# Kernel tuning notes

Hardware: AMD Instinct MI355X
Metric: run time of the kernel (lower is better)

Reference implementation:

```python
import jax, jax.numpy as jnp
import numpy as np

NUM_HEADS = 12
EPS = 1e-6


def setup_inputs() -> dict:
    key = jax.random.key(0)
    k1, k2, k3, k4 = jax.random.split(key, 4)
    N, B, D = 1025, 8, 768
    x = jax.random.normal(k1, (N, B, D), dtype=jnp.float32)
    # torch nn.Linear weights: [out_features, in_features]
    w_qkv = jax.random.normal(k2, (3 * D, D), dtype=jnp.float32) * (D ** -0.5)
    w_proj = jax.random.normal(k3, (D, D), dtype=jnp.float32) * (D ** -0.5)
    b_proj = jax.random.normal(k4, (D,), dtype=jnp.float32) * 0.01
    return {"x": x, "w_qkv": w_qkv, "w_proj": w_proj, "b_proj": b_proj}


def reference(x, w_qkv, w_proj, b_proj):
    N, B, D = x.shape
    H = NUM_HEADS
    hd = D // H
    scale = hd ** -0.5
    scale_vv = scale * 1.0  # scale_multiplier = 1.0

    xb = jnp.transpose(x, (1, 0, 2))  # [B, N, D]
    qkv = xb @ w_qkv.T  # [B, N, 3D]
    qkv = qkv.reshape(B, N, 3, H, hd).transpose(2, 0, 3, 1, 4)  # [3, B, H, N, hd]
    q, k, v = qkv[0], qkv[1], qkv[2]

    # QK path: only row 0 of out_ori survives the masking, compute just that row
    scores0 = jnp.einsum('bhqd,bhkd->bhqk', q[:, :, :1], k) * scale  # [B,H,1,N]
    attn0 = jax.nn.softmax(scores0, axis=-1)
    out0 = jnp.einsum('bhqk,bhkd->bhqd', attn0, v)  # [B,H,1,hd]

    # VV cosine path: only rows 1: survive
    vn = v / jnp.maximum(jnp.linalg.norm(v, axis=-1, keepdims=True), EPS)
    scores_vv = jnp.einsum('bhqd,bhkd->bhqk', vn[:, :, 1:], vn) * scale_vv  # [B,H,N-1,N]
    attn_vv = jax.nn.softmax(scores_vv, axis=-1)
    out_vv = jnp.einsum('bhqk,bhkd->bhqd', attn_vv, v)  # [B,H,N-1,hd]

    out = jnp.concatenate([out0, out_vv], axis=2)  # [B,H,N,hd]
    out = out.transpose(0, 2, 1, 3).reshape(B, N, D)
    out = out @ w_proj.T + b_proj
    return jnp.transpose(out, (1, 0, 2))  # [N, B, D]
```

## Files before the change

kernel.cpp:

```cpp
#include <hip/hip_runtime.h>

typedef unsigned short u16;
typedef unsigned int   u32;
typedef __attribute__((ext_vector_type(8))) short short8;
typedef __attribute__((ext_vector_type(4))) float f32x4;

#define AS1 __attribute__((address_space(1)))
#define AS3 __attribute__((address_space(3)))

#define NSEQ  1025
#define BB    8
#define DD    768
#define HH    12
#define MROWS 8200
#define MPAD  8320
#define KPAD  1088

__device__ __forceinline__ void gl2lds16(const void* g, void* l) {
  __builtin_amdgcn_global_load_lds((const AS1 u32*)g, (AS3 u32*)l, 16, 0, 0);
}
__device__ __forceinline__ u16 f2bf(float f) {
  u32 u = __float_as_uint(f);
  return (u16)((u + 0x7FFFu + ((u >> 16) & 1u)) >> 16);
}
__device__ __forceinline__ float bf2f(u16 u) { return __uint_as_float(((u32)u) << 16); }

__global__ __launch_bounds__(256) void prep(const float* __restrict__ x,
                                            const float* __restrict__ wqkv,
                                            const float* __restrict__ wproj,
                                            u16* __restrict__ xb,
                                            u16* __restrict__ wkv,
                                            u16* __restrict__ wpj) {
  const int XB_G  = MPAD * 192;
  const int WKV_G = 1536 * 192;
  const int WPJ_G = 768 * 192;
  int g = blockIdx.x * 256 + threadIdx.x;
  float4 v;
  u16* dst;
  size_t di;
  if (g < XB_G) {
    int m = g / 192, e4 = g - m * 192;
    if (m < MROWS) {
      int bb = m / NSEQ, ns = m - bb * NSEQ;
      v = ((const float4*)x)[(size_t)(ns * BB + bb) * 192 + e4];
    } else {
      v.x = v.y = v.z = v.w = 0.f;
    }
    dst = xb; di = (size_t)g;
  } else if (g < XB_G + WKV_G) {
    int r = g - XB_G;
    v = ((const float4*)wqkv)[(size_t)147456 + r];
    dst = wkv; di = (size_t)r;
  } else if (g < XB_G + WKV_G + WPJ_G) {
    int r = g - XB_G - WKV_G;
    v = ((const float4*)wproj)[r];
    dst = wpj; di = (size_t)r;
  } else {
    return;
  }
  uint2 o;
  o.x = (u32)f2bf(v.x) | ((u32)f2bf(v.y) << 16);
  o.y = (u32)f2bf(v.z) | ((u32)f2bf(v.w) << 16);
  ((uint2*)dst)[di] = o;
}

template <int MODE, int NT>
__global__ __launch_bounds__(256) void gemm_bt(const u16* __restrict__ A,
                                               const u16* __restrict__ W,
                                               u16* __restrict__ Cbf,
                                               float* __restrict__ Cf,
                                               const float* __restrict__ bias,
                                               int ldc) {
  __shared__ u16 sA[128 * 64];
  __shared__ u16 sW[128 * 64];
  const int id = blockIdx.x;
  const int rx = id & 7, qx = id >> 3;
  const int kq = qx / NT;
  const int m_t = rx + (kq << 3);
  if (m_t > 64) return;
  const int n_t = qx - kq * NT;
  const int m0 = m_t << 7, n0 = n_t << 7;

  const int tid = threadIdx.x;
  const int w = tid >> 6, lane = tid & 63;
  const int wm = w & 1, wn = w >> 1;
  const int lc = lane & 15, lr = lane >> 4;

  f32x4 zero4 = {0.f, 0.f, 0.f, 0.f};
  f32x4 acc[4][4];
#pragma unroll
  for (int i = 0; i < 4; ++i)
#pragma unroll
    for (int j = 0; j < 4; ++j) acc[i][j] = zero4;

  const int r0 = tid >> 3;
  const int ko = (tid & 7) << 3;
  const u16* gA = A + (size_t)(m0 + r0) * DD + ko;
  const u16* gW = W + (size_t)(n0 + r0) * DD + ko;
  char* lA = (char*)sA + tid * 16;
  char* lW = (char*)sW + tid * 16;

#pragma unroll 1
  for (int kt = 0; kt < 12; ++kt) {
    __syncthreads();
#pragma unroll
    for (int j = 0; j < 4; ++j) {
      gl2lds16(gA + (size_t)j * 32 * DD + kt * 64, lA + j * 4096);
      gl2lds16(gW + (size_t)j * 32 * DD + kt * 64, lW + j * 4096);
    }
    __syncthreads();
#pragma unroll
    for (int kk = 0; kk < 2; ++kk) {
      short8 af[4], wf[4];
#pragma unroll
      for (int mt = 0; mt < 4; ++mt)
        af[mt] = *(const short8*)((char*)sA + ((wm << 6) + (mt << 4) + lc) * 128 + (kk << 6) + (lr << 4));
#pragma unroll
      for (int nt = 0; nt < 4; ++nt)
        wf[nt] = *(const short8*)((char*)sW + ((wn << 6) + (nt << 4) + lc) * 128 + (kk << 6) + (lr << 4));
#pragma unroll
      for (int mt = 0; mt < 4; ++mt)
#pragma unroll
        for (int nt = 0; nt < 4; ++nt)
          acc[mt][nt] = __builtin_amdgcn_mfma_f32_16x16x32_bf16(af[mt], wf[nt], acc[mt][nt], 0, 0, 0);
    }
  }

  if (MODE == 0) {
#pragma unroll
    for (int mt = 0; mt < 4; ++mt)
#pragma unroll
      for (int r = 0; r < 4; ++r) {
        int m = m0 + (wm << 6) + (mt << 4) + (lr << 2) + r;
        if (m < MROWS) {
          size_t base = (size_t)m * ldc + n0 + (wn << 6) + lc;
#pragma unroll
          for (int nt = 0; nt < 4; ++nt) Cbf[base + (nt << 4)] = f2bf(acc[mt][nt][r]);
        }
      }
  } else {
    float b4[4];
#pragma unroll
    for (int nt = 0; nt < 4; ++nt) b4[nt] = bias[n0 + (wn << 6) + (nt << 4) + lc];
#pragma unroll
    for (int mt = 0; mt < 4; ++mt)
#pragma unroll
      for (int r = 0; r < 4; ++r) {
        int m = m0 + (wm << 6) + (mt << 4) + (lr << 2) + r;
        if (m < MROWS) {
          int bb = m / NSEQ;
          int ns = m - bb * NSEQ;
          float* o = Cf + (size_t)ns * (BB * DD) + bb * DD + n0 + (wn << 6) + lc;
#pragma unroll
          for (int nt = 0; nt < 4; ++nt) o[nt << 4] = acc[mt][nt][r] + b4[nt];
        }
      }
  }
}

__global__ __launch_bounds__(256) void q0_kernel(const float* __restrict__ x,
                                                 const float* __restrict__ wq,
                                                 float* __restrict__ q0) {
  __shared__ float red[256];
  int bid = blockIdx.x;
  int b = bid / HH, c = bid - b * HH;
  int tid = threadIdx.x;
  int dp = (c << 6) + (tid >> 2), part = tid & 3;
  const float4* x4 = (const float4*)(x + (size_t)b * DD + part * 192);
  const float4* w4 = (const float4*)(wq + (size_t)dp * DD + part * 192);
  float acc = 0.f;
#pragma unroll 4
  for (int e = 0; e < 48; ++e) {
    float4 a = x4[e], w = w4[e];
    acc += a.x * w.x + a.y * w.y + a.z * w.z + a.w * w.w;
  }
  red[tid] = acc;
  __syncthreads();
  if (part == 0) q0[b * DD + dp] = red[tid] + red[tid + 1] + red[tid + 2] + red[tid + 3];
}

__global__ __launch_bounds__(256) void transpose_v(const u16* __restrict__ kv,
                                                   u16* __restrict__ vT,
                                                   u16* __restrict__ vn) {
  __shared__ u16 tile[64][72];
  __shared__ float red[256];
  __shared__ float sInv[64];
  int bid = blockIdx.x;
  int kc = bid % 17;
  int t2 = bid / 17;
  int h = t2 % HH, b = t2 / HH;
  int tid = threadIdx.x;
  int kl = tid >> 2, dc = (tid & 3) << 4;
  int key = kc * 64 + kl;
  u32 vals[8];
  if (key < NSEQ) {
    const u32* g = (const u32*)(kv + ((size_t)b * NSEQ + key) * 1536 + DD + h * 64 + dc);
#pragma unroll
    for (int i = 0; i < 8; ++i) vals[i] = g[i];
  } else {
#pragma unroll
    for (int i = 0; i < 8; ++i) vals[i] = 0;
  }
  float part = 0.f;
#pragma unroll
  for (int i = 0; i < 8; ++i) {
    float a = bf2f((u16)(vals[i] & 0xFFFF));
    float c = bf2f((u16)(vals[i] >> 16));
    part += a * a + c * c;
    ((u32*)&tile[kl][dc])[i] = vals[i];
  }
  red[tid] = part;
  __syncthreads();
  if ((tid & 3) == 0) {
    float s = red[tid] + red[tid + 1] + red[tid + 2] + red[tid + 3];
    sInv[kl] = (key < NSEQ) ? 1.0f / fmaxf(sqrtf(s), 1e-6f) : 0.0f;
  }
  __syncthreads();
  float iv = sInv[kl];
  u32 ovn[8];
#pragma unroll
  for (int i = 0; i < 8; ++i) {
    float a = bf2f((u16)(vals[i] & 0xFFFF)) * iv;
    float c = bf2f((u16)(vals[i] >> 16)) * iv;
    ovn[i] = (u32)f2bf(a) | ((u32)f2bf(c) << 16);
  }
  u32* on = (u32*)(vn + ((size_t)(b * HH + h) * KPAD + key) * 64 + dc);
#pragma unroll
  for (int i = 0; i < 8; ++i) on[i] = ovn[i];
  int dl = tid >> 2, ks = (tid & 3) << 4;
  u32 ov[8];
#pragma unroll
  for (int i = 0; i < 8; ++i)
    ov[i] = (u32)tile[ks + 2 * i][dl] | ((u32)tile[ks + 2 * i + 1][dl] << 16);
  u16* o = vT + (size_t)(b * HH + h) * 64 * KPAD + (size_t)dl * KPAD + kc * 64 + ks;
#pragma unroll
  for (int i = 0; i < 8; ++i) ((u32*)o)[i] = ov[i];
}

__global__ __launch_bounds__(256) void row0_attn(const float* __restrict__ q0,
                                                 const u16* __restrict__ kv,
                                                 u16* __restrict__ attn) {
  __shared__ float sq[64];
  __shared__ float sc[NSEQ];
  __shared__ float red[256];
  __shared__ float rpv[32][68];
  int bid = blockIdx.x;
  int b = bid / HH, h = bid - b * HH;
  int tid = threadIdx.x;
  if (tid < 64) sq[tid] = q0[b * DD + h * 64 + tid];
  __syncthreads();
  float mx = -1e30f;
  for (int n = tid; n < NSEQ; n += 256) {
    const u32* kr = (const u32*)(kv + ((size_t)b * NSEQ + n) * 1536 + h * 64);
    float s = 0.f;
#pragma unroll
    for (int i = 0; i < 32; ++i) {
      u32 u = kr[i];
      s += bf2f((u16)(u & 0xFFFF)) * sq[2 * i] + bf2f((u16)(u >> 16)) * sq[2 * i + 1];
    }
    s *= 0.125f;
    sc[n] = s;
    mx = fmaxf(mx, s);
  }
  red[tid] = mx;
  __syncthreads();
  for (int st = 128; st > 0; st >>= 1) {
    if (tid < st) red[tid] = fmaxf(red[tid], red[tid + st]);
    __syncthreads();
  }
  mx = red[0];
  __syncthreads();
  float ds = 0.f;
  for (int n = tid; n < NSEQ; n += 256) {
    float p = __expf(sc[n] - mx);
    sc[n] = p;
    ds += p;
  }
  red[tid] = ds;
  __syncthreads();
  for (int st = 128; st > 0; st >>= 1) {
    if (tid < st) red[tid] += red[tid + st];
    __syncthreads();
  }
  float den = red[0];
  __syncthreads();

  int kp = tid >> 3, dc = (tid & 7) << 3;
  const u16* vb = kv + (size_t)b * NSEQ * 1536 + DD + h * 64 + dc;
  float acc[8];
#pragma unroll
  for (int i = 0; i < 8; ++i) acc[i] = 0.f;
#pragma unroll 4
  for (int j = 0; j < 32; ++j) {
    int n = kp + (j << 5);
    uint4 v = *(const uint4*)(vb + (size_t)n * 1536);
    float p = sc[n];
    acc[0] += p * bf2f((u16)(v.x & 0xFFFF));
    acc[1] += p * bf2f((u16)(v.x >> 16));
    acc[2] += p * bf2f((u16)(v.y & 0xFFFF));
    acc[3] += p * bf2f((u16)(v.y >> 16));
    acc[4] += p * bf2f((u16)(v.z & 0xFFFF));
    acc[5] += p * bf2f((u16)(v.z >> 16));
    acc[6] += p * bf2f((u16)(v.w & 0xFFFF));
    acc[7] += p * bf2f((u16)(v.w >> 16));
  }
  if (kp == 0) {
    uint4 v = *(const uint4*)(vb + (size_t)1024 * 1536);
    float p = sc[1024];
    acc[0] += p * bf2f((u16)(v.x & 0xFFFF));
    acc[1] += p * bf2f((u16)(v.x >> 16));
    acc[2] += p * bf2f((u16)(v.y & 0xFFFF));
    acc[3] += p * bf2f((u16)(v.y >> 16));
    acc[4] += p * bf2f((u16)(v.z & 0xFFFF));
    acc[5] += p * bf2f((u16)(v.z >> 16));
    acc[6] += p * bf2f((u16)(v.w & 0xFFFF));
    acc[7] += p * bf2f((u16)(v.w >> 16));
  }
#pragma unroll
  for (int i = 0; i < 8; ++i) rpv[kp][dc + i] = acc[i];
  __syncthreads();
  if (tid < 64) {
    float s = 0.f;
#pragma unroll
    for (int p = 0; p < 32; ++p) s += rpv[p][tid];
    attn[(size_t)b * NSEQ * DD + h * 64 + tid] = f2bf(s / den);
  }
}

__global__ __launch_bounds__(256) void vv_attn(const u16* __restrict__ vn,
                                               const u16* __restrict__ vT,
                                               u16* __restrict__ attn) {
  __shared__ u16 sQ[2 * 128 * 32];
  __shared__ u16 sK[2 * 64 * 32];
  __shared__ u16 sV[2 * 64 * 32];
  __shared__ u16 sP[128 * 72];

  const int tid = threadIdx.x, w = tid >> 6, lane = tid & 63;
  const int lc = lane & 15, lr = lane >> 4;
  const int bh = blockIdx.x;
  const int m0 = blockIdx.y << 7;
  const int b = bh / HH, h = bh - b * HH;
  const char* nb = (const char*)(vn + (size_t)bh * KPAD * 64);
  const char* tb = (const char*)(vT + (size_t)bh * 64 * KPAD);

#pragma unroll
  for (int j = 0; j < 4; ++j) {
    int lin = (w << 12) + (j << 10) + (lane << 4);
    int hf = lin >> 13, r = (lin >> 6) & 127, off = lin & 63;
    gl2lds16(nb + (size_t)(1 + m0 + r) * 128 + hf * 64 + off, (char*)sQ + lin);
  }

  f32x4 zero4 = {0.f, 0.f, 0.f, 0.f};
  f32x4 oacc[2][4];
  f32x4 dacc[2];
#pragma unroll
  for (int i = 0; i < 2; ++i) {
    dacc[i] = zero4;
#pragma unroll
    for (int j = 0; j < 4; ++j) oacc[i][j] = zero4;
  }
  short8 ones;
#pragma unroll
  for (int i = 0; i < 8; ++i) ones[i] = (short)0x3F80;

  const float CEXP = 0.1803368801111204f;

#pragma unroll 1
  for (int kt = 0; kt < 17; ++kt) {
    __syncthreads();
#pragma unroll
    for (int j = 0; j < 2; ++j) {
      int lin = (w << 11) + (j << 10) + (lane << 4);
      int hf = lin >> 12, r = (lin >> 6) & 63, off = lin & 63;
      gl2lds16(nb + (size_t)(kt * 64 + r) * 128 + hf * 64 + off, (char*)sK + lin);
      gl2lds16(tb + (size_t)r * (KPAD * 2) + kt * 128 + hf * 64 + off, (char*)sV + lin);
    }
    __syncthreads();

    f32x4 sacc[4][2];
#pragma unroll
    for (int mt = 0; mt < 4; ++mt)
#pragma unroll
      for (int nt = 0; nt < 2; ++nt) sacc[mt][nt] = zero4;
#pragma unroll
    for (int kk = 0; kk < 2; ++kk) {
      short8 ak[4], bq[2];
#pragma unroll
      for (int mt = 0; mt < 4; ++mt)
        ak[mt] = *(const short8*)((char*)sK + (kk << 12) + ((mt << 4) + lc) * 64 + (lr << 4));
#pragma unroll
      for (int nt = 0; nt < 2; ++nt)
        bq[nt] = *(const short8*)((char*)sQ + (kk << 13) + ((w << 5) + (nt << 4) + lc) * 64 + (lr << 4));
#pragma unroll
      for (int mt = 0; mt < 4; ++mt)
#pragma unroll
        for (int nt = 0; nt < 2; ++nt)
          sacc[mt][nt] = __builtin_amdgcn_mfma_f32_16x16x32_bf16(ak[mt], bq[nt], sacc[mt][nt], 0, 0, 0);
    }

#pragma unroll
    for (int mt = 0; mt < 4; ++mt) {
      int kl0 = (mt << 4) + (lr << 2);
#pragma unroll
      for (int nt = 0; nt < 2; ++nt) {
        int q = (w << 5) + (nt << 4) + lc;
        u32 a0 = __float_as_uint(__builtin_amdgcn_exp2f(sacc[mt][nt][0] * CEXP)) + 0x8000u;
        u32 a1 = __float_as_uint(__builtin_amdgcn_exp2f(sacc[mt][nt][1] * CEXP)) + 0x8000u;
        u32 a2 = __float_as_uint(__builtin_amdgcn_exp2f(sacc[mt][nt][2] * CEXP)) + 0x8000u;
        u32 a3 = __float_as_uint(__builtin_amdgcn_exp2f(sacc[mt][nt][3] * CEXP)) + 0x8000u;
        uint2 pv;
        pv.x = __builtin_amdgcn_perm(a1, a0, 0x07060302u);
        pv.y = __builtin_amdgcn_perm(a3, a2, 0x07060302u);
        if (kt == 16) {
          pv.x = (kl0 == 0) ? (pv.x & 0xFFFFu) : 0u;
          pv.y = 0u;
        }
        *(uint2*)((char*)sP + q * 144 + (kl0 << 1)) = pv;
      }
    }

#pragma unroll
    for (int kk = 0; kk < 2; ++kk) {
      short8 ap[2], bv[4];
#pragma unroll
      for (int mt = 0; mt < 2; ++mt)
        ap[mt] = *(const short8*)((char*)sP + ((w << 5) + (mt << 4) + lc) * 144 + (kk << 6) + (lr << 4));
#pragma unroll
      for (int nt = 0; nt < 4; ++nt)
        bv[nt] = *(const short8*)((char*)sV + (kk << 12) + ((nt << 4) + lc) * 64 + (lr << 4));
#pragma unroll
      for (int mt = 0; mt < 2; ++mt) {
#pragma unroll
        for (int nt = 0; nt < 4; ++nt)
          oacc[mt][nt] = __builtin_amdgcn_mfma_f32_16x16x32_bf16(ap[mt], bv[nt], oacc[mt][nt], 0, 0, 0);
        dacc[mt] = __builtin_amdgcn_mfma_f32_16x16x32_bf16(ap[mt], ones, dacc[mt], 0, 0, 0);
      }
    }
  }

#pragma unroll
  for (int mt = 0; mt < 2; ++mt) {
#pragma unroll
    for (int r = 0; r < 4; ++r) {
      int q = (w << 5) + (mt << 4) + (lr << 2) + r;
      int nseq = 1 + m0 + q;
      float rdn = 1.0f / dacc[mt][r];
      size_t obase = ((size_t)b * NSEQ + nseq) * DD + h * 64 + lc;
#pragma unroll
      for (int nt = 0; nt < 4; ++nt) attn[obase + (nt << 4)] = f2bf(oacc[mt][nt][r] * rdn);
    }
  }
}

extern "C" void kernel_launch(void* const* d_in, const int* in_sizes, int n_in,
                              void* d_out, int out_size, void* d_ws, size_t ws_size,
                              hipStream_t stream) {
  const float* x      = (const float*)d_in[0];
  const float* w_qkv  = (const float*)d_in[1];
  const float* w_proj = (const float*)d_in[2];
  const float* b_proj = (const float*)d_in[3];
  float* out = (float*)d_out;
  char* ws = (char*)d_ws;

  u16*   xb   = (u16*)(ws + 0);
  u16*   vT   = (u16*)(ws + 0);
  u16*   wkv  = (u16*)(ws + 13369344);
  u16*   wpj  = (u16*)(ws + 15728640);
  u16*   kvb  = (u16*)(ws + 16908288);
  float* q0   = (float*)(ws + 42467328);
  u16*   attn = (u16*)(ws + 42491904);
  u16*   vn   = (u16*)(ws + 55271424);

  prep<<<7968, 256, 0, stream>>>(x, w_qkv, w_proj, xb, wkv, wpj);
  gemm_bt<0, 12><<<864, 256, 0, stream>>>(xb, wkv, kvb, nullptr, nullptr, 1536);
  q0_kernel<<<96, 256, 0, stream>>>(x, w_qkv, q0);
  transpose_v<<<1632, 256, 0, stream>>>(kvb, vT, vn);
  row0_attn<<<96, 256, 0, stream>>>(q0, kvb, attn);
  vv_attn<<<dim3(96, 8), 256, 0, stream>>>(vn, vT, attn);
  gemm_bt<1, 6><<<432, 256, 0, stream>>>(attn, wpj, nullptr, out, b_proj, 768);
}
```

Measured before the change: 222.5 us.

## Swizzle LDS tiles into MFMA fragment order and split P·V into halves

Rearranges the Q, K, V and P tiles in shared memory so each lane reads its MFMA fragment as one contiguous 16-byte chunk. This is meant to remove LDS bank conflicts and per-iteration address arithmetic, and the global-to-LDS source and destination pointers are now precomputed outside the loop. The P tile shrinks to a per-wave half-tile that is written and consumed in two halves, and the last half-tile is skipped at the tail iteration. A launch-bounds occupancy hint of 4 is added, which may force register spilling.

```diff
diff --git a/kernel.cpp b/kernel.cpp
--- a/kernel.cpp
+++ b/kernel.cpp
@@ -327,13 +327,13 @@
   }
 }
 
-__global__ __launch_bounds__(256) void vv_attn(const u16* __restrict__ vn,
-                                               const u16* __restrict__ vT,
-                                               u16* __restrict__ attn) {
-  __shared__ u16 sQ[2 * 128 * 32];
-  __shared__ u16 sK[2 * 64 * 32];
-  __shared__ u16 sV[2 * 64 * 32];
-  __shared__ u16 sP[128 * 72];
+__global__ __launch_bounds__(256, 4) void vv_attn(const u16* __restrict__ vn,
+                                                  const u16* __restrict__ vT,
+                                                  u16* __restrict__ attn) {
+  __shared__ u16 sQ[2 * 8 * 64 * 8];
+  __shared__ u16 sK[2 * 4 * 64 * 8];
+  __shared__ u16 sV[2 * 4 * 64 * 8];
+  __shared__ u16 sP[4 * 2 * 64 * 8];
 
   const int tid = threadIdx.x, w = tid >> 6, lane = tid & 63;
   const int lc = lane & 15, lr = lane >> 4;
@@ -346,8 +346,25 @@
 #pragma unroll
   for (int j = 0; j < 4; ++j) {
     int lin = (w << 12) + (j << 10) + (lane << 4);
-    int hf = lin >> 13, r = (lin >> 6) & 127, off = lin & 63;
-    gl2lds16(nb + (size_t)(1 + m0 + r) * 128 + hf * 64 + off, (char*)sQ + lin);
+    int kk = lin >> 13, qg = (lin >> 10) & 7;
+    int lr2 = (lin >> 8) & 3, lc2 = (lin >> 4) & 15;
+    gl2lds16(nb + (size_t)(1 + m0 + (qg << 4) + lc2) * 128 + (kk << 6) + (lr2 << 4),
+             (char*)sQ + lin);
+  }
+
+  const char* srcK[2];
+  const char* srcV[2];
+  char* dstK[2];
+  char* dstV[2];
+#pragma unroll
+  for (int j = 0; j < 2; ++j) {
+    int lin = (w << 11) + (j << 10) + (lane << 4);
+    int kk = lin >> 12, kg = (lin >> 10) & 3;
+    int lr2 = (lin >> 8) & 3, lc2 = (lin >> 4) & 15;
+    srcK[j] = nb + (size_t)((kg << 4) + lc2) * 128 + (kk << 6) + (lr2 << 4);
+    srcV[j] = tb + (size_t)((kg << 4) + lc2) * (KPAD * 2) + (kk << 6) + (lr2 << 4);
+    dstK[j] = (char*)sK + lin;
+    dstV[j] = (char*)sV + lin;
   }
 
   f32x4 zero4 = {0.f, 0.f, 0.f, 0.f};
@@ -365,15 +382,19 @@
 
   const float CEXP = 0.1803368801111204f;
 
+  const char* rdK = (const char*)sK + (lane << 4);
+  const char* rdQ = (const char*)sQ + ((w << 1) << 10) + (lane << 4);
+  const char* rdV = (const char*)sV + (lane << 4);
+  const char* rdP = (const char*)sP + (w << 11) + (lane << 4);
+  char* wrP = (char*)sP + (w << 11) + ((lr >> 1) << 8) + (lc << 4) + ((lr & 1) << 3);
+
 #pragma unroll 1
   for (int kt = 0; kt < 17; ++kt) {
     __syncthreads();
 #pragma unroll
     for (int j = 0; j < 2; ++j) {
-      int lin = (w << 11) + (j << 10) + (lane << 4);
-      int hf = lin >> 12, r = (lin >> 6) & 63, off = lin & 63;
-      gl2lds16(nb + (size_t)(kt * 64 + r) * 128 + hf * 64 + off, (char*)sK + lin);
-      gl2lds16(tb + (size_t)r * (KPAD * 2) + kt * 128 + hf * 64 + off, (char*)sV + lin);
+      gl2lds16(srcK[j] + (size_t)kt * 8192, dstK[j]);
+      gl2lds16(srcV[j] + (size_t)kt * 128, dstV[j]);
     }
     __syncthreads();
 
@@ -387,10 +408,10 @@
       short8 ak[4], bq[2];
 #pragma unroll
       for (int mt = 0; mt < 4; ++mt)
-        ak[mt] = *(const short8*)((char*)sK + (kk << 12) + ((mt << 4) + lc) * 64 + (lr << 4));
+        ak[mt] = *(const short8*)(rdK + (kk << 12) + (mt << 10));
 #pragma unroll
       for (int nt = 0; nt < 2; ++nt)
-        bq[nt] = *(const short8*)((char*)sQ + (kk << 13) + ((w << 5) + (nt << 4) + lc) * 64 + (lr << 4));
+        bq[nt] = *(const short8*)(rdQ + (kk << 13) + (nt << 10));
 #pragma unroll
       for (int mt = 0; mt < 4; ++mt)
 #pragma unroll
@@ -399,41 +420,45 @@
     }
 
 #pragma unroll
-    for (int mt = 0; mt < 4; ++mt) {
-      int kl0 = (mt << 4) + (lr << 2);
-#pragma unroll
-      for (int nt = 0; nt < 2; ++nt) {
-        int q = (w << 5) + (nt << 4) + lc;
-        u32 a0 = __float_as_uint(__builtin_amdgcn_exp2f(sacc[mt][nt][0] * CEXP)) + 0x8000u;
-        u32 a1 = __float_as_uint(__builtin_amdgcn_exp2f(sacc[mt][nt][1] * CEXP)) + 0x8000u;
-        u32 a2 = __float_as_uint(__builtin_amdgcn_exp2f(sacc[mt][nt][2] * CEXP)) + 0x8000u;
-        u32 a3 = __float_as_uint(__builtin_amdgcn_exp2f(sacc[mt][nt][3] * CEXP)) + 0x8000u;
-        uint2 pv;
-        pv.x = __builtin_amdgcn_perm(a1, a0, 0x07060302u);
-        pv.y = __builtin_amdgcn_perm(a3, a2, 0x07060302u);
-        if (kt == 16) {
-          pv.x = (kl0 == 0) ? (pv.x & 0xFFFFu) : 0u;
-          pv.y = 0u;
+    for (int h2 = 0; h2 < 2; ++h2) {
+      if (!(kt == 16 && h2 == 1)) {
+        asm volatile("" ::: "memory");
+#pragma unroll
+        for (int mi = 0; mi < 2; ++mi) {
+          int ms = (h2 << 1) + mi;
+#pragma unroll
+          for (int nt = 0; nt < 2; ++nt) {
+            f32x4 s = sacc[ms][nt];
+            u32 a0 = __float_as_uint(__builtin_amdgcn_exp2f(s[0] * CEXP)) + 0x8000u;
+            u32 a1 = __float_as_uint(__builtin_amdgcn_exp2f(s[1] * CEXP)) + 0x8000u;
+            u32 a2 = __float_as_uint(__builtin_amdgcn_exp2f(s[2] * CEXP)) + 0x8000u;
+            u32 a3 = __float_as_uint(__builtin_amdgcn_exp2f(s[3] * CEXP)) + 0x8000u;
+            uint2 pv;
+            pv.x = __builtin_amdgcn_perm(a1, a0, 0x07060302u);
+            pv.y = __builtin_amdgcn_perm(a3, a2, 0x07060302u);
+            if (kt == 16) {
+              pv.x = (ms == 0 && lr == 0) ? (pv.x & 0xFFFFu) : 0u;
+              pv.y = 0u;
+            }
+            *(uint2*)(wrP + (nt << 10) + (mi << 9)) = pv;
+          }
         }
-        *(uint2*)((char*)sP + q * 144 + (kl0 << 1)) = pv;
-      }
-    }
-
-#pragma unroll
-    for (int kk = 0; kk < 2; ++kk) {
-      short8 ap[2], bv[4];
-#pragma unroll
-      for (int mt = 0; mt < 2; ++mt)
-        ap[mt] = *(const short8*)((char*)sP + ((w << 5) + (mt << 4) + lc) * 144 + (kk << 6) + (lr << 4));
-#pragma unroll
-      for (int nt = 0; nt < 4; ++nt)
-        bv[nt] = *(const short8*)((char*)sV + (kk << 12) + ((nt << 4) + lc) * 64 + (lr << 4));
-#pragma unroll
-      for (int mt = 0; mt < 2; ++mt) {
+        __builtin_amdgcn_sched_barrier(0);
+        asm volatile("" ::: "memory");
+        short8 ap[2], bv[4];
+#pragma unroll
+        for (int mt = 0; mt < 2; ++mt)
+          ap[mt] = *(const short8*)(rdP + (mt << 10));
 #pragma unroll
         for (int nt = 0; nt < 4; ++nt)
-          oacc[mt][nt] = __builtin_amdgcn_mfma_f32_16x16x32_bf16(ap[mt], bv[nt], oacc[mt][nt], 0, 0, 0);
-        dacc[mt] = __builtin_amdgcn_mfma_f32_16x16x32_bf16(ap[mt], ones, dacc[mt], 0, 0, 0);
+          bv[nt] = *(const short8*)(rdV + (h2 << 12) + (nt << 10));
+#pragma unroll
+        for (int mt = 0; mt < 2; ++mt) {
+#pragma unroll
+          for (int nt = 0; nt < 4; ++nt)
+            oacc[mt][nt] = __builtin_amdgcn_mfma_f32_16x16x32_bf16(ap[mt], bv[nt], oacc[mt][nt], 0, 0, 0);
+          dacc[mt] = __builtin_amdgcn_mfma_f32_16x16x32_bf16(ap[mt], ones, dacc[mt], 0, 0, 0);
+        }
       }
     }
   }
```

Result: no change. 219.4 us (-1.4%).
